# Kernel optimization log

Hardware: AMD Instinct MI355X
Metric: run time of the kernel (lower is better)

The kernel has to match this reference:

```python
import jax, jax.numpy as jnp
import numpy as np

NUM_HEADS = 8
EPS = 1e-6


def conv1x1(x, w, b):
    # x: [b,c,h,w], w: [out,in], b: [out]  (torch Conv2d 1x1 weight squeezed)
    return jnp.einsum('bchw,oc->bohw', x, w) + b[None, :, None, None]


def feature_map(x):
    return jax.nn.elu(x) + 1.0


def setup_inputs() -> dict:
    key = jax.random.key(0)
    ks = jax.random.split(key, 9)
    C = 512
    s = 1.0 / np.sqrt(C)
    x = jax.random.normal(ks[0], (8, C, 64, 64), dtype=jnp.float32)
    wq = jax.random.normal(ks[1], (C, C), dtype=jnp.float32) * s
    wk = jax.random.normal(ks[2], (C, C), dtype=jnp.float32) * s
    wv = jax.random.normal(ks[3], (C, C), dtype=jnp.float32) * s
    wo = jax.random.normal(ks[4], (C, C), dtype=jnp.float32) * s
    bq = jax.random.normal(ks[5], (C,), dtype=jnp.float32) * 0.01
    bk = jax.random.normal(ks[6], (C,), dtype=jnp.float32) * 0.01
    bv = jax.random.normal(ks[7], (C,), dtype=jnp.float32) * 0.01
    bo = jax.random.normal(ks[8], (C,), dtype=jnp.float32) * 0.01
    return {'x': x, 'wq': wq, 'bq': bq, 'wk': wk, 'bk': bk,
            'wv': wv, 'bv': bv, 'wo': wo, 'bo': bo}


def reference(x, wq, bq, wk, bk, wv, bv, wo, bo):
    b, c, h, w = x.shape
    nh = NUM_HEADS
    hd = c // nh
    L = h * w

    def to_heads(t):
        # [b,c,h,w] -> [b,nh,L,hd]
        return t.reshape(b, nh, hd, L).transpose(0, 1, 3, 2)

    Q = feature_map(to_heads(conv1x1(x, wq, bq)))
    K = feature_map(to_heads(conv1x1(x, wk, bk)))
    V = to_heads(conv1x1(x, wv, bv)) / L  # values / v_length

    KV = jnp.einsum('bhld,bhlv->bhdv', K, V)                 # [b,nh,hd,hd]
    Z = 1.0 / (jnp.einsum('bhld,bhd->bhl', Q, K.sum(axis=-2)) + EPS)
    out = jnp.einsum('bhld,bhdv,bhl->bhlv', Q, KV, Z) * L    # [b,nh,L,hd]

    out = out.transpose(0, 1, 3, 2).reshape(b, c, h, w)
    return conv1x1(out, wo, bo)
```

## Files before the change

kernel.cpp:

```cpp
#include <hip/hip_runtime.h>
#include <hip/hip_bf16.h>

#define BATCH 8
#define CCH   512
#define NHD   8
#define HD    64
#define LLEN  4096
#define M1    1536

typedef __bf16 bf16x8 __attribute__((ext_vector_type(8)));
typedef __bf16 bf16x4 __attribute__((ext_vector_type(4)));
typedef float  f32x4  __attribute__((ext_vector_type(4)));

__device__ __forceinline__ f32x4 mfma16(bf16x8 a, bf16x8 b, f32x4 c) {
  return __builtin_amdgcn_mfma_f32_16x16x32_bf16(a, b, c, 0, 0, 0);
}

__global__ void pack_w(const float* __restrict__ wq, const float* __restrict__ wk,
                       const float* __restrict__ wv, const float* __restrict__ wo,
                       const float* __restrict__ bq, const float* __restrict__ bk,
                       const float* __restrict__ bv,
                       __bf16* __restrict__ wqkvb, __bf16* __restrict__ wob,
                       float* __restrict__ biasq) {
  const int n = M1 * CCH + CCH * CCH + M1;
  for (int i = blockIdx.x * blockDim.x + threadIdx.x; i < n; i += gridDim.x * blockDim.x) {
    if (i < M1 * CCH) {
      int r = i >> 9, c = i & 511;
      float v = (r < 512) ? wq[r * 512 + c]
              : (r < 1024) ? wk[(r - 512) * 512 + c]
                           : wv[(r - 1024) * 512 + c];
      wqkvb[i] = (__bf16)v;
    } else if (i < M1 * CCH + CCH * CCH) {
      int j = i - M1 * CCH;
      wob[j] = (__bf16)wo[j];
    } else {
      int j = i - M1 * CCH - CCH * CCH;
      biasq[j] = (j < 512) ? bq[j] : (j < 1024) ? bk[j - 512] : bv[j - 1024];
    }
  }
}

__global__ void transpose_x(const float* __restrict__ x, __bf16* __restrict__ xt) {
  __shared__ float tile[32][33];
  const int b = blockIdx.z, c0 = blockIdx.y * 32, l0 = blockIdx.x * 32;
  const int tx = threadIdx.x & 31, ty = threadIdx.x >> 5;
  const float* xp = x + ((size_t)b * CCH + c0) * LLEN + l0;
#pragma unroll
  for (int j = 0; j < 4; ++j)
    tile[ty + j * 8][tx] = xp[(size_t)(ty + j * 8) * LLEN + tx];
  __syncthreads();
  __bf16* xo = xt + ((size_t)b * LLEN + l0) * CCH + c0;
#pragma unroll
  for (int j = 0; j < 4; ++j)
    xo[(size_t)(ty + j * 8) * CCH + tx] = (__bf16)tile[tx][ty + j * 8];
}

template <int EPI>
__global__ __launch_bounds__(256) void gemm_k(
    const __bf16* __restrict__ A, const __bf16* __restrict__ Bm,
    const float* __restrict__ bias,
    __bf16* __restrict__ qt, __bf16* __restrict__ kcm, __bf16* __restrict__ vcm,
    float* __restrict__ out) {
  __shared__ __attribute__((aligned(16))) __bf16 As[128 * 36];
  __shared__ __attribute__((aligned(16))) __bf16 Bs[128 * 36];
  const int b  = blockIdx.z;
  const int n0 = blockIdx.x * 128;
  const int m0 = blockIdx.y * 128;
  const int tid = threadIdx.x;
  const int ll = tid & 63, w = tid >> 6;
  const int wr = w >> 1, wc = w & 1;
  const int lhi = ll >> 4, llo = ll & 15;

  const __bf16* Bp = Bm + ((size_t)b * LLEN + n0) * CCH;

  f32x4 acc[4][4];
#pragma unroll
  for (int i = 0; i < 4; ++i)
#pragma unroll
    for (int j = 0; j < 4; ++j) acc[i][j] = (f32x4){0.f, 0.f, 0.f, 0.f};

  for (int kt = 0; kt < 16; ++kt) {
    const int k0 = kt * 32;
    if (kt) __syncthreads();
#pragma unroll
    for (int j = 0; j < 2; ++j) {
      int idx = tid + j * 256;
      int row = idx >> 2, c8 = (idx & 3) * 8;
      bf16x8 va = *(const bf16x8*)(A + (size_t)(m0 + row) * CCH + k0 + c8);
      *(bf16x4*)(As + row * 36 + c8)     = ((bf16x4*)&va)[0];
      *(bf16x4*)(As + row * 36 + c8 + 4) = ((bf16x4*)&va)[1];
      bf16x8 vb = *(const bf16x8*)(Bp + (size_t)row * CCH + k0 + c8);
      *(bf16x4*)(Bs + row * 36 + c8)     = ((bf16x4*)&vb)[0];
      *(bf16x4*)(Bs + row * 36 + c8 + 4) = ((bf16x4*)&vb)[1];
    }
    __syncthreads();
    bf16x8 af[4], bfr[4];
#pragma unroll
    for (int i = 0; i < 4; ++i) {
      const __bf16* pa = As + (wr * 64 + i * 16 + llo) * 36 + lhi * 8;
      ((bf16x4*)&af[i])[0] = *(const bf16x4*)pa;
      ((bf16x4*)&af[i])[1] = *(const bf16x4*)(pa + 4);
      const __bf16* pb = Bs + (wc * 64 + i * 16 + llo) * 36 + lhi * 8;
      ((bf16x4*)&bfr[i])[0] = *(const bf16x4*)pb;
      ((bf16x4*)&bfr[i])[1] = *(const bf16x4*)(pb + 4);
    }
#pragma unroll
    for (int i = 0; i < 4; ++i)
#pragma unroll
      for (int j = 0; j < 4; ++j) acc[i][j] = mfma16(af[i], bfr[j], acc[i][j]);
  }

#pragma unroll
  for (int i = 0; i < 4; ++i) {
    const int o0 = m0 + wr * 64 + i * 16 + lhi * 4;
#pragma unroll
    for (int j = 0; j < 4; ++j) {
      const int col = n0 + wc * 64 + j * 16 + llo;
      if (EPI == 0) {
        if (m0 < 512) {
          bf16x4 pk;
#pragma unroll
          for (int r = 0; r < 4; ++r) {
            float t = acc[i][j][r] + bias[o0 + r];
            t = t > 0.f ? t + 1.f : __expf(t);
            pk[r] = (__bf16)t;
          }
          *(bf16x4*)(qt + ((size_t)b * LLEN + col) * CCH + o0) = pk;
        } else if (m0 < 1024) {
#pragma unroll
          for (int r = 0; r < 4; ++r) {
            float t = acc[i][j][r] + bias[o0 + r];
            t = t > 0.f ? t + 1.f : __expf(t);
            kcm[((size_t)b * CCH + (o0 - 512 + r)) * LLEN + col] = (__bf16)t;
          }
        } else {
#pragma unroll
          for (int r = 0; r < 4; ++r)
            vcm[((size_t)b * CCH + (o0 - 1024 + r)) * LLEN + col] =
                (__bf16)(acc[i][j][r] + bias[o0 + r]);
        }
      } else {
#pragma unroll
        for (int r = 0; r < 4; ++r)
          out[((size_t)b * CCH + o0 + r) * LLEN + col] = acc[i][j][r] + bias[o0 + r];
      }
    }
  }
}

__global__ void ksum_k(const __bf16* __restrict__ kcm, float* __restrict__ ksum) {
  const int bid = blockIdx.x;
  const __bf16* p = kcm + (size_t)bid * LLEN;
  const int t = threadIdx.x;
  float s = 0.f;
  bf16x8 v0 = *(const bf16x8*)(p + t * 16);
  bf16x8 v1 = *(const bf16x8*)(p + t * 16 + 8);
#pragma unroll
  for (int i = 0; i < 8; ++i) s += (float)v0[i] + (float)v1[i];
  for (int off = 32; off; off >>= 1) s += __shfl_down(s, off);
  __shared__ float sw[4];
  if ((t & 63) == 0) sw[t >> 6] = s;
  __syncthreads();
  if (t == 0) ksum[bid] = sw[0] + sw[1] + sw[2] + sw[3];
}

__global__ __launch_bounds__(64) void kv_part_k(const __bf16* __restrict__ kcm,
                                                const __bf16* __restrict__ vcm,
                                                float* __restrict__ part) {
  const int lc = blockIdx.x, bh = blockIdx.y;
  const int b = bh >> 3, h = bh & 7;
  const int ll = threadIdx.x, lhi = ll >> 4, llo = ll & 15;
  const __bf16* Kp = kcm + ((size_t)b * CCH + h * 64) * LLEN;
  const __bf16* Vp = vcm + ((size_t)b * CCH + h * 64) * LLEN;
  f32x4 acc[4][4];
#pragma unroll
  for (int i = 0; i < 4; ++i)
#pragma unroll
    for (int j = 0; j < 4; ++j) acc[i][j] = (f32x4){0.f, 0.f, 0.f, 0.f};
  const int base = lc * 512 + lhi * 8;
  for (int kt = 0; kt < 16; ++kt) {
    const int k0 = base + kt * 32;
    bf16x8 af[4], bfr[4];
#pragma unroll
    for (int i = 0; i < 4; ++i) af[i]  = *(const bf16x8*)(Kp + (size_t)(i * 16 + llo) * LLEN + k0);
#pragma unroll
    for (int i = 0; i < 4; ++i) bfr[i] = *(const bf16x8*)(Vp + (size_t)(i * 16 + llo) * LLEN + k0);
#pragma unroll
    for (int i = 0; i < 4; ++i)
#pragma unroll
      for (int j = 0; j < 4; ++j) acc[i][j] = mfma16(af[i], bfr[j], acc[i][j]);
  }
  float* op = part + ((size_t)lc * 64 + bh) * 4096;
#pragma unroll
  for (int i = 0; i < 4; ++i)
#pragma unroll
    for (int j = 0; j < 4; ++j)
#pragma unroll
      for (int r = 0; r < 4; ++r) {
        int d = i * 16 + lhi * 4 + r, v = j * 16 + llo;
        op[d * 64 + v] = acc[i][j][r];
      }
}

__global__ void kv_red_k(const float* __restrict__ part, float* __restrict__ kv) {
  const int i = blockIdx.x * blockDim.x + threadIdx.x;
  float s = 0.f;
#pragma unroll
  for (int lc = 0; lc < 8; ++lc) s += part[(size_t)lc * 262144 + i];
  kv[i] = s;
}

__global__ __launch_bounds__(256) void apply_k(const __bf16* __restrict__ qt,
                                               const float* __restrict__ kv,
                                               const float* __restrict__ ksum,
                                               __bf16* __restrict__ attn) {
  __shared__ __attribute__((aligned(16))) __bf16 kvT[64 * 68];
  __shared__ float zb[256];
  const int lc = blockIdx.x, bh = blockIdx.y;
  const int b = bh >> 3, h = bh & 7;
  const int tid = threadIdx.x;
  const float* kvp = kv + (size_t)bh * 4096;
  for (int i = tid; i < 4096; i += 256) {
    int d = i >> 6, v = i & 63;
    kvT[v * 68 + d] = (__bf16)kvp[i];
  }
  const int l = lc * 256 + tid;
  const __bf16* qp = qt + ((size_t)b * LLEN + l) * CCH + h * 64;
  const float* ksp = ksum + bh * 64;
  float s = 0.f;
#pragma unroll
  for (int d8 = 0; d8 < 64; d8 += 8) {
    bf16x8 qv = *(const bf16x8*)(qp + d8);
#pragma unroll
    for (int i = 0; i < 8; ++i) s += (float)qv[i] * ksp[d8 + i];
  }
  zb[tid] = 1.0f / (s + 1e-6f);
  __syncthreads();

  const int ll = tid & 63, w = tid >> 6, lhi = ll >> 4, llo = ll & 15;
  f32x4 acc[4][4];
#pragma unroll
  for (int i = 0; i < 4; ++i)
#pragma unroll
    for (int j = 0; j < 4; ++j) acc[i][j] = (f32x4){0.f, 0.f, 0.f, 0.f};
  const __bf16* qbase = qt + ((size_t)b * LLEN + lc * 256 + w * 64) * CCH + h * 64;
#pragma unroll
  for (int kt = 0; kt < 2; ++kt) {
    const int k8 = kt * 32 + lhi * 8;
    bf16x8 af[4], bfr[4];
#pragma unroll
    for (int i = 0; i < 4; ++i)
      af[i] = *(const bf16x8*)(qbase + (size_t)(i * 16 + llo) * CCH + k8);
#pragma unroll
    for (int j = 0; j < 4; ++j) {
      const __bf16* pb = kvT + (j * 16 + llo) * 68 + k8;
      ((bf16x4*)&bfr[j])[0] = *(const bf16x4*)pb;
      ((bf16x4*)&bfr[j])[1] = *(const bf16x4*)(pb + 4);
    }
#pragma unroll
    for (int i = 0; i < 4; ++i)
#pragma unroll
      for (int j = 0; j < 4; ++j) acc[i][j] = mfma16(af[i], bfr[j], acc[i][j]);
  }
  __bf16* ap = attn + ((size_t)b * LLEN + lc * 256) * CCH + h * 64;
#pragma unroll
  for (int i = 0; i < 4; ++i)
#pragma unroll
    for (int j = 0; j < 4; ++j)
#pragma unroll
      for (int r = 0; r < 4; ++r) {
        int ml = w * 64 + i * 16 + lhi * 4 + r;
        int v = j * 16 + llo;
        ap[(size_t)ml * CCH + v] = (__bf16)(acc[i][j][r] * zb[ml]);
      }
}

extern "C" void kernel_launch(void* const* d_in, const int* in_sizes, int n_in,
                              void* d_out, int out_size, void* d_ws, size_t ws_size,
                              hipStream_t stream) {
  const float* x  = (const float*)d_in[0];
  const float* wq = (const float*)d_in[1];
  const float* bq = (const float*)d_in[2];
  const float* wk = (const float*)d_in[3];
  const float* bk = (const float*)d_in[4];
  const float* wv = (const float*)d_in[5];
  const float* bv = (const float*)d_in[6];
  const float* wo = (const float*)d_in[7];
  const float* bo = (const float*)d_in[8];
  float* out = (float*)d_out;

  char* p = (char*)d_ws;
  __bf16* xt    = (__bf16*)p; p += (size_t)BATCH * LLEN * CCH * 2;
  __bf16* qt    = (__bf16*)p; p += (size_t)BATCH * LLEN * CCH * 2;
  __bf16* kcm   = (__bf16*)p; p += (size_t)BATCH * CCH * LLEN * 2;
  __bf16* vcm   = (__bf16*)p; p += (size_t)BATCH * CCH * LLEN * 2;
  __bf16* wqkvb = (__bf16*)p; p += (size_t)M1 * CCH * 2;
  __bf16* wob   = (__bf16*)p; p += (size_t)CCH * CCH * 2;
  float*  biasq = (float*)p;  p += (size_t)M1 * 4;
  float*  ksum  = (float*)p;  p += (size_t)BATCH * CCH * 4;
  float*  part  = (float*)p;  p += (size_t)8 * 64 * HD * HD * 4;
  float*  kvb   = (float*)p;  p += (size_t)64 * HD * HD * 4;
  __bf16* attn  = xt;

  pack_w<<<1024, 256, 0, stream>>>(wq, wk, wv, wo, bq, bk, bv, wqkvb, wob, biasq);
  transpose_x<<<dim3(128, 16, BATCH), 256, 0, stream>>>(x, xt);
  gemm_k<0><<<dim3(32, 12, BATCH), 256, 0, stream>>>(wqkvb, xt, biasq, qt, kcm, vcm, nullptr);
  ksum_k<<<4096, 256, 0, stream>>>(kcm, ksum);
  kv_part_k<<<dim3(8, 64), 64, 0, stream>>>(kcm, vcm, part);
  kv_red_k<<<1024, 256, 0, stream>>>(part, kvb);
  apply_k<<<dim3(16, 64), 256, 0, stream>>>(qt, kvb, ksum, attn);
  gemm_k<1><<<dim3(32, 4, BATCH), 256, 0, stream>>>(wob, attn, bo, nullptr, nullptr, nullptr, out);
}
```

Baseline: 187.8 us.

## Use direct global-to-LDS loads in GEMM, widen transpose, fuse key-sum into KV

The GEMM staging now uses global_load_lds with 16-byte transfers, writing tiles straight into unpadded shared memory and reading fragments as single 16-byte loads. The x transpose moves to 64x64 tiles with float4 reads and 4-wide bf16 writes. The separate key-sum kernel is removed: kv_part_k accumulates per-row K sums alongside the MFMA work, and a small reduction kernel combines the partials. The intent is to cut memory traffic and launch count, at the risk of LDS bank conflicts from dropping the row padding.

Result: faster. 172.9 us (-7.9%).

```diff
diff --git a/kernel.cpp b/kernel.cpp
--- a/kernel.cpp
+++ b/kernel.cpp
@@ -1,5 +1,6 @@
 #include <hip/hip_runtime.h>
 #include <hip/hip_bf16.h>
+#include <stdint.h>
 
 #define BATCH 8
 #define CCH   512
@@ -14,6 +15,13 @@
 
 __device__ __forceinline__ f32x4 mfma16(bf16x8 a, bf16x8 b, f32x4 c) {
   return __builtin_amdgcn_mfma_f32_16x16x32_bf16(a, b, c, 0, 0, 0);
+}
+
+__device__ __forceinline__ void gload_lds16(const void* g, void* l) {
+  __builtin_amdgcn_global_load_lds(
+      (const __attribute__((address_space(1))) uint32_t*)(uintptr_t)g,
+      (__attribute__((address_space(3))) uint32_t*)(uintptr_t)l,
+      16, 0, 0);
 }
 
 __global__ void pack_w(const float* __restrict__ wq, const float* __restrict__ wk,
@@ -40,19 +48,33 @@
   }
 }
 
-__global__ void transpose_x(const float* __restrict__ x, __bf16* __restrict__ xt) {
-  __shared__ float tile[32][33];
-  const int b = blockIdx.z, c0 = blockIdx.y * 32, l0 = blockIdx.x * 32;
-  const int tx = threadIdx.x & 31, ty = threadIdx.x >> 5;
+__global__ __launch_bounds__(256) void transpose_x(const float* __restrict__ x,
+                                                   __bf16* __restrict__ xt) {
+  __shared__ float tile[64][65];
+  const int b = blockIdx.z, c0 = blockIdx.y * 64, l0 = blockIdx.x * 64;
+  const int t = threadIdx.x;
+  const int lq = (t & 15) * 4, cr = t >> 4;
   const float* xp = x + ((size_t)b * CCH + c0) * LLEN + l0;
 #pragma unroll
-  for (int j = 0; j < 4; ++j)
-    tile[ty + j * 8][tx] = xp[(size_t)(ty + j * 8) * LLEN + tx];
+  for (int q = 0; q < 4; ++q) {
+    const int c = cr + q * 16;
+    float4 v = *(const float4*)(xp + (size_t)c * LLEN + lq);
+    tile[c][lq + 0] = v.x;
+    tile[c][lq + 1] = v.y;
+    tile[c][lq + 2] = v.z;
+    tile[c][lq + 3] = v.w;
+  }
   __syncthreads();
   __bf16* xo = xt + ((size_t)b * LLEN + l0) * CCH + c0;
-#pragma unroll
-  for (int j = 0; j < 4; ++j)
-    xo[(size_t)(ty + j * 8) * CCH + tx] = (__bf16)tile[tx][ty + j * 8];
+  const int c4 = (t & 15) * 4, lr = t >> 4;
+#pragma unroll
+  for (int p = 0; p < 4; ++p) {
+    const int l = lr + p * 16;
+    bf16x4 o;
+#pragma unroll
+    for (int i = 0; i < 4; ++i) o[i] = (__bf16)tile[c4 + i][l];
+    *(bf16x4*)(xo + (size_t)l * CCH + c4) = o;
+  }
 }
 
 template <int EPI>
@@ -61,8 +83,8 @@
     const float* __restrict__ bias,
     __bf16* __restrict__ qt, __bf16* __restrict__ kcm, __bf16* __restrict__ vcm,
     float* __restrict__ out) {
-  __shared__ __attribute__((aligned(16))) __bf16 As[128 * 36];
-  __shared__ __attribute__((aligned(16))) __bf16 Bs[128 * 36];
+  __shared__ __attribute__((aligned(16))) __bf16 As[128 * 32];
+  __shared__ __attribute__((aligned(16))) __bf16 Bs[128 * 32];
   const int b  = blockIdx.z;
   const int n0 = blockIdx.x * 128;
   const int m0 = blockIdx.y * 128;
@@ -70,7 +92,9 @@
   const int ll = tid & 63, w = tid >> 6;
   const int wr = w >> 1, wc = w & 1;
   const int lhi = ll >> 4, llo = ll & 15;
-
+  const int r4 = ll >> 2, c8e = (ll & 3) * 8;
+
+  const __bf16* Ap = A + (size_t)m0 * CCH;
   const __bf16* Bp = Bm + ((size_t)b * LLEN + n0) * CCH;
 
   f32x4 acc[4][4];
@@ -83,26 +107,17 @@
     const int k0 = kt * 32;
     if (kt) __syncthreads();
 #pragma unroll
-    for (int j = 0; j < 2; ++j) {
-      int idx = tid + j * 256;
-      int row = idx >> 2, c8 = (idx & 3) * 8;
-      bf16x8 va = *(const bf16x8*)(A + (size_t)(m0 + row) * CCH + k0 + c8);
-      *(bf16x4*)(As + row * 36 + c8)     = ((bf16x4*)&va)[0];
-      *(bf16x4*)(As + row * 36 + c8 + 4) = ((bf16x4*)&va)[1];
-      bf16x8 vb = *(const bf16x8*)(Bp + (size_t)row * CCH + k0 + c8);
-      *(bf16x4*)(Bs + row * 36 + c8)     = ((bf16x4*)&vb)[0];
-      *(bf16x4*)(Bs + row * 36 + c8 + 4) = ((bf16x4*)&vb)[1];
+    for (int i = 0; i < 2; ++i) {
+      const int rb = i * 64 + w * 16;
+      gload_lds16(Ap + (size_t)(rb + r4) * CCH + k0 + c8e, As + rb * 32);
+      gload_lds16(Bp + (size_t)(rb + r4) * CCH + k0 + c8e, Bs + rb * 32);
     }
     __syncthreads();
     bf16x8 af[4], bfr[4];
 #pragma unroll
     for (int i = 0; i < 4; ++i) {
-      const __bf16* pa = As + (wr * 64 + i * 16 + llo) * 36 + lhi * 8;
-      ((bf16x4*)&af[i])[0] = *(const bf16x4*)pa;
-      ((bf16x4*)&af[i])[1] = *(const bf16x4*)(pa + 4);
-      const __bf16* pb = Bs + (wc * 64 + i * 16 + llo) * 36 + lhi * 8;
-      ((bf16x4*)&bfr[i])[0] = *(const bf16x4*)pb;
-      ((bf16x4*)&bfr[i])[1] = *(const bf16x4*)(pb + 4);
+      af[i]  = *(const bf16x8*)(As + (wr * 64 + i * 16 + llo) * 32 + lhi * 8);
+      bfr[i] = *(const bf16x8*)(Bs + (wc * 64 + i * 16 + llo) * 32 + lhi * 8);
     }
 #pragma unroll
     for (int i = 0; i < 4; ++i)
@@ -148,25 +163,10 @@
   }
 }
 
-__global__ void ksum_k(const __bf16* __restrict__ kcm, float* __restrict__ ksum) {
-  const int bid = blockIdx.x;
-  const __bf16* p = kcm + (size_t)bid * LLEN;
-  const int t = threadIdx.x;
-  float s = 0.f;
-  bf16x8 v0 = *(const bf16x8*)(p + t * 16);
-  bf16x8 v1 = *(const bf16x8*)(p + t * 16 + 8);
-#pragma unroll
-  for (int i = 0; i < 8; ++i) s += (float)v0[i] + (float)v1[i];
-  for (int off = 32; off; off >>= 1) s += __shfl_down(s, off);
-  __shared__ float sw[4];
-  if ((t & 63) == 0) sw[t >> 6] = s;
-  __syncthreads();
-  if (t == 0) ksum[bid] = sw[0] + sw[1] + sw[2] + sw[3];
-}
-
 __global__ __launch_bounds__(64) void kv_part_k(const __bf16* __restrict__ kcm,
                                                 const __bf16* __restrict__ vcm,
-                                                float* __restrict__ part) {
+                                                float* __restrict__ part,
+                                                float* __restrict__ part_ks) {
   const int lc = blockIdx.x, bh = blockIdx.y;
   const int b = bh >> 3, h = bh & 7;
   const int ll = threadIdx.x, lhi = ll >> 4, llo = ll & 15;
@@ -177,6 +177,7 @@
   for (int i = 0; i < 4; ++i)
 #pragma unroll
     for (int j = 0; j < 4; ++j) acc[i][j] = (f32x4){0.f, 0.f, 0.f, 0.f};
+  float ks[4] = {0.f, 0.f, 0.f, 0.f};
   const int base = lc * 512 + lhi * 8;
   for (int kt = 0; kt < 16; ++kt) {
     const int k0 = base + kt * 32;
@@ -188,6 +189,10 @@
 #pragma unroll
     for (int i = 0; i < 4; ++i)
 #pragma unroll
+      for (int r = 0; r < 8; ++r) ks[i] += (float)af[i][r];
+#pragma unroll
+    for (int i = 0; i < 4; ++i)
+#pragma unroll
       for (int j = 0; j < 4; ++j) acc[i][j] = mfma16(af[i], bfr[j], acc[i][j]);
   }
   float* op = part + ((size_t)lc * 64 + bh) * 4096;
@@ -200,6 +205,14 @@
         int d = i * 16 + lhi * 4 + r, v = j * 16 + llo;
         op[d * 64 + v] = acc[i][j][r];
       }
+  float* pks = part_ks + ((size_t)lc * 64 + bh) * 64;
+#pragma unroll
+  for (int i = 0; i < 4; ++i) {
+    float s = ks[i];
+    s += __shfl_xor(s, 16);
+    s += __shfl_xor(s, 32);
+    if (lhi == 0) pks[i * 16 + llo] = s;
+  }
 }
 
 __global__ void kv_red_k(const float* __restrict__ part, float* __restrict__ kv) {
@@ -208,6 +221,14 @@
 #pragma unroll
   for (int lc = 0; lc < 8; ++lc) s += part[(size_t)lc * 262144 + i];
   kv[i] = s;
+}
+
+__global__ void ksum_red_k(const float* __restrict__ part_ks, float* __restrict__ ksum) {
+  const int i = blockIdx.x * blockDim.x + threadIdx.x;
+  float s = 0.f;
+#pragma unroll
+  for (int lc = 0; lc < 8; ++lc) s += part_ks[(size_t)lc * 4096 + i];
+  ksum[i] = s;
 }
 
 __global__ __launch_bounds__(256) void apply_k(const __bf16* __restrict__ qt,
@@ -300,14 +321,15 @@
   float*  ksum  = (float*)p;  p += (size_t)BATCH * CCH * 4;
   float*  part  = (float*)p;  p += (size_t)8 * 64 * HD * HD * 4;
   float*  kvb   = (float*)p;  p += (size_t)64 * HD * HD * 4;
+  float*  pks   = (float*)p;  p += (size_t)8 * 64 * 64 * 4;
   __bf16* attn  = xt;
 
   pack_w<<<1024, 256, 0, stream>>>(wq, wk, wv, wo, bq, bk, bv, wqkvb, wob, biasq);
-  transpose_x<<<dim3(128, 16, BATCH), 256, 0, stream>>>(x, xt);
+  transpose_x<<<dim3(64, 8, BATCH), 256, 0, stream>>>(x, xt);
   gemm_k<0><<<dim3(32, 12, BATCH), 256, 0, stream>>>(wqkvb, xt, biasq, qt, kcm, vcm, nullptr);
-  ksum_k<<<4096, 256, 0, stream>>>(kcm, ksum);
-  kv_part_k<<<dim3(8, 64), 64, 0, stream>>>(kcm, vcm, part);
+  kv_part_k<<<dim3(8, 64), 64, 0, stream>>>(kcm, vcm, part, pks);
   kv_red_k<<<1024, 256, 0, stream>>>(part, kvb);
+  ksum_red_k<<<16, 256, 0, stream>>>(pks, ksum);
   apply_k<<<dim3(16, 64), 256, 0, stream>>>(qt, kvb, ksum, attn);
   gemm_k<1><<<dim3(32, 4, BATCH), 256, 0, stream>>>(wob, attn, bo, nullptr, nullptr, nullptr, out);
 }
```
